# Optimization experiments

Measured on AMD Instinct MI355X. Metric: run time of the kernel, lower is better.

The kernel has to match this reference:

```python
import jax, jax.numpy as jnp
import numpy as np

N, E = 50000, 800000
HID, EDGE_DIM, HEADS = 128, 16, 4
C = HID // HEADS  # 32
NEG_SLOPE = 0.2  # GATv2Conv default negative_slope


def setup_inputs() -> dict:
    key = jax.random.key(0)
    ks = jax.random.split(key, 16)
    def glorot(k, shape):
        fan_in = shape[0]
        return jax.random.normal(k, shape, jnp.float32) / np.sqrt(fan_in)
    return {
        "x": jax.random.normal(ks[0], (N, HID), jnp.float32),
        "edge_index": jax.random.randint(ks[1], (2, E), 0, N, jnp.int64 if jax.config.jax_enable_x64 else jnp.int32),
        "edge_attr": jax.random.normal(ks[2], (E, EDGE_DIM), jnp.float32),
        # GATv2Conv params (lin_l, lin_r with bias; lin_edge bias-free; att; final bias)
        "Wl": glorot(ks[3], (HID, HID)),
        "bl": jnp.zeros((HID,), jnp.float32),
        "Wr": glorot(ks[4], (HID, HID)),
        "br": jnp.zeros((HID,), jnp.float32),
        "We": glorot(ks[5], (EDGE_DIM, HID)),
        "att": glorot(ks[6], (HEADS, C)),
        "bias_gat": jnp.zeros((HID,), jnp.float32),
        # RMSNorm weights
        "w_norm1": jnp.ones((HID,), jnp.float32),
        "w_norm2": jnp.ones((HID,), jnp.float32),
        # FFN params
        "ffn_w1": glorot(ks[7], (HID, 4 * HID)),
        "ffn_b1": jnp.zeros((4 * HID,), jnp.float32),
        "ffn_w2": glorot(ks[8], (4 * HID, HID)),
        "ffn_b2": jnp.zeros((HID,), jnp.float32),
    }


def rmsnorm(x, w):
    # torch.nn.RMSNorm with eps=None -> eps = finfo(dtype).eps
    eps = jnp.finfo(x.dtype).eps
    ms = jnp.mean(x * x, axis=-1, keepdims=True)
    return x * jax.lax.rsqrt(ms + eps) * w


def gatv2_conv(x, edge_index, edge_attr, Wl, bl, Wr, br, We, att, bias_gat):
    n = x.shape[0]
    h, c = att.shape
    xl = (x @ Wl + bl).reshape(n, h, c)   # source-side transform (x_j)
    xr = (x @ Wr + br).reshape(n, h, c)   # target-side transform (x_i)
    src, dst = edge_index[0], edge_index[1]
    e = (edge_attr @ We).reshape(-1, h, c)
    m = xl[src] + xr[dst] + e                       # [E, H, C] per-edge message pre-activation
    s = jnp.where(m > 0, m, NEG_SLOPE * m)          # LeakyReLU(0.2)
    logits = jnp.einsum('ehc,hc->eh', s, att)       # [E, H]
    # scatter-softmax over edges grouped by target node
    lmax = jax.ops.segment_max(logits, dst, num_segments=n)
    ex = jnp.exp(logits - lmax[dst])
    den = jax.ops.segment_sum(ex, dst, num_segments=n)
    alpha = ex / (den[dst] + 1e-16)                 # PyG softmax denominator guard
    out = jax.ops.segment_sum(alpha[..., None] * xl[src], dst, num_segments=n)
    return out.reshape(n, h * c) + bias_gat


def reference(x, edge_index, edge_attr, Wl, bl, Wr, br, We, att, bias_gat,
              w_norm1, w_norm2, ffn_w1, ffn_b1, ffn_w2, ffn_b2):
    x_attn = gatv2_conv(x, edge_index, edge_attr, Wl, bl, Wr, br, We, att, bias_gat)
    h = rmsnorm(x + x_attn, w_norm1)
    f = jax.nn.gelu(h @ ffn_w1 + ffn_b1, approximate=False) @ ffn_w2 + ffn_b2
    return rmsnorm(h + f, w_norm2)
```

## Files before the change

### kernel.cpp

```cpp
#include <hip/hip_runtime.h>

#define NN 50000
#define EE 800000

typedef unsigned short u16;

#define OFF_EAH  0u
#define OFF_XLH  6400000u
#define OFF_XRH  9600000u
#define OFF_SE   12800000u
#define OFF_CNT  14400000u
#define OFF_OFS  14450000u
#define OFF_WLRT 16000000u
#define OFF_W1T  16016384u
#define OFF_W2T  16049152u

#define RMS_EPS 1.1920928955078125e-7f

typedef float f32x4v __attribute__((ext_vector_type(4)));
typedef short s16x8 __attribute__((ext_vector_type(8)));
typedef _Float16 h16x2 __attribute__((ext_vector_type(2)));
typedef __fp16   g16x2 __attribute__((ext_vector_type(2)));

__device__ __forceinline__ f32x4v mfma16(s16x8 a, s16x8 b, f32x4v c) {
  return __builtin_amdgcn_mfma_f32_16x16x32_bf16(a, b, c, 0, 0, 0);
}
__device__ __forceinline__ u16 f2b(float f) {
  unsigned int u = __float_as_uint(f);
  unsigned int r = (u + 0x7fffu + ((u >> 16) & 1u)) >> 16;
  return (u16)r;
}
__device__ __forceinline__ u16 f2h(float f) {
  union { _Float16 h; u16 u; } x; x.h = (_Float16)f; return x.u;
}
__device__ __forceinline__ h16x2 pk(float a, float b) {
  union { g16x2 g; h16x2 h; } u; u.g = __builtin_amdgcn_cvt_pkrtz(a, b); return u.h;
}
__device__ __forceinline__ h16x2 u2h(unsigned int u) {
  union { unsigned int i; h16x2 h; } x; x.i = u; return x.h;
}
__device__ __forceinline__ unsigned int h2u(h16x2 h) {
  union { unsigned int i; h16x2 h; } x; x.h = h; return x.i;
}
__device__ __forceinline__ float fdot2(h16x2 a, h16x2 b, float c) {
  union { h16x2 h; g16x2 g; } ua, ub; ua.h = a; ub.h = b;
  return __builtin_amdgcn_fdot2(ua.g, ub.g, c, false);
}
__device__ __forceinline__ s16x8 ld_bf16x8_f32(const float* p) {
  float4 v0 = *(const float4*)p;
  float4 v1 = *(const float4*)(p + 4);
  s16x8 r;
  r[0] = (short)f2b(v0.x); r[1] = (short)f2b(v0.y);
  r[2] = (short)f2b(v0.z); r[3] = (short)f2b(v0.w);
  r[4] = (short)f2b(v1.x); r[5] = (short)f2b(v1.y);
  r[6] = (short)f2b(v1.z); r[7] = (short)f2b(v1.w);
  return r;
}
__device__ __forceinline__ int readlane_i32(int v, int lane) {
  return __builtin_amdgcn_readlane(v, lane);
}
__device__ __forceinline__ float gelu_fast(float x) {
  float x2 = x * x;
  float y = x * fmaf(0.07135481283f, x2, 1.5957691216f);
  float e = __expf(-y);
  return x * __builtin_amdgcn_rcpf(1.0f + e);
}

__global__ __launch_bounds__(256) void k_prep(const float* __restrict__ Wl, const float* __restrict__ Wr,
    const float* __restrict__ W1, const float* __restrict__ W2,
    int* __restrict__ cnt, u16* __restrict__ wlrt, u16* __restrict__ w1t, u16* __restrict__ w2t)
{
  int i = blockIdx.x * 256 + threadIdx.x;
  if (i < NN) cnt[i] = 0;
  if (i < 32768) {
    int n = i >> 7, k = i & 127;
    float v = (n < 128) ? Wl[k * 128 + n] : Wr[k * 128 + (n - 128)];
    wlrt[i] = f2b(v);
  }
  {
    int n = i >> 7, k = i & 127;
    w1t[i] = f2b(W1[k * 512 + n]);
  }
  {
    int n = i >> 9, k = i & 511;
    w2t[i] = f2b(W2[k * 128 + n]);
  }
}

__global__ __launch_bounds__(256) void k_hist(const int* __restrict__ ei, const float* __restrict__ eattr,
    int* __restrict__ cnt, unsigned int* __restrict__ eah)
{
  int e = blockIdx.x * 256 + threadIdx.x;
  if (e < EE) {
    atomicAdd(&cnt[ei[EE + e]], 1);
    const float4* src = (const float4*)(eattr + (size_t)e * 16);
    float4 v0 = src[0], v1 = src[1], v2 = src[2], v3 = src[3];
    uint4 o0, o1;
    o0.x = h2u(pk(v0.x, v0.y));
    o0.y = h2u(pk(v0.z, v0.w));
    o0.z = h2u(pk(v1.x, v1.y));
    o0.w = h2u(pk(v1.z, v1.w));
    o1.x = h2u(pk(v2.x, v2.y));
    o1.y = h2u(pk(v2.z, v2.w));
    o1.z = h2u(pk(v3.x, v3.y));
    o1.w = h2u(pk(v3.z, v3.w));
    uint4* dst = (uint4*)(eah + (size_t)e * 8);
    dst[0] = o0; dst[1] = o1;
  }
}

#define SCAN_PER 49
__global__ __launch_bounds__(1024) void k_scan(const int* __restrict__ cnt,
    int* __restrict__ offs, int* __restrict__ pos)
{
  __shared__ int wsum[16];
  int tid = threadIdx.x, lane = tid & 63, wv = tid >> 6;
  int base = tid * SCAN_PER;
  int v[SCAN_PER];
  int s = 0;
#pragma unroll
  for (int i = 0; i < SCAN_PER; ++i) {
    int idx = base + i;
    v[i] = (idx < NN) ? cnt[idx] : 0;
    s += v[i];
  }
  int x = s;
#pragma unroll
  for (int o = 1; o < 64; o <<= 1) {
    int y = __shfl_up(x, o);
    if (lane >= o) x += y;
  }
  if (lane == 63) wsum[wv] = x;
  __syncthreads();
  if (wv == 0) {
    int t = (lane < 16) ? wsum[lane] : 0;
#pragma unroll
    for (int o = 1; o < 16; o <<= 1) {
      int y = __shfl_up(t, o);
      if (lane >= o) t += y;
    }
    if (lane < 16) wsum[lane] = t;
  }
  __syncthreads();
  int wbase = (wv > 0) ? wsum[wv - 1] : 0;
  int run = x - s + wbase;
#pragma unroll
  for (int i = 0; i < SCAN_PER; ++i) {
    int idx = base + i;
    if (idx < NN) {
      pos[idx] = run;
      run += v[i];
      offs[idx + 1] = run;
    }
  }
  if (tid == 0) offs[0] = 0;
}

__global__ __launch_bounds__(256) void k_permute(const int* __restrict__ ei,
    int* __restrict__ pos, int2* __restrict__ se)
{
  int e = blockIdx.x * 256 + threadIdx.x;
  if (e < EE) {
    int slot = atomicAdd(&pos[ei[EE + e]], 1);
    se[slot] = make_int2(ei[e], e);
  }
}

__global__ __launch_bounds__(256) void k1_mfma(const float* __restrict__ x, const u16* __restrict__ wlrt,
    const float* __restrict__ bl, const float* __restrict__ br,
    u16* __restrict__ xlh, u16* __restrict__ xrh)
{
  int tid = threadIdx.x;
  int w = tid >> 6, lane = tid & 63;
  int quad = lane >> 4, l16 = lane & 15;
  int row0 = blockIdx.x * 32;
  int ko = quad * 8;
  f32x4v acc[2][4];
#pragma unroll
  for (int mt = 0; mt < 2; ++mt)
#pragma unroll
    for (int nt = 0; nt < 4; ++nt) acc[mt][nt] = (f32x4v){0.f, 0.f, 0.f, 0.f};
#pragma unroll
  for (int ks = 0; ks < 4; ++ks) {
    int k0 = ks * 32 + ko;
    s16x8 a[2];
#pragma unroll
    for (int mt = 0; mt < 2; ++mt) {
      int row = row0 + mt * 16 + l16; if (row >= NN) row = NN - 1;
      a[mt] = ld_bf16x8_f32(x + row * 128 + k0);
    }
#pragma unroll
    for (int nt = 0; nt < 4; ++nt) {
      int col = w * 64 + nt * 16 + l16;
      s16x8 b = *(const s16x8*)(wlrt + col * 128 + k0);
      acc[0][nt] = mfma16(a[0], b, acc[0][nt]);
      acc[1][nt] = mfma16(a[1], b, acc[1][nt]);
    }
  }
#pragma unroll
  for (int nt = 0; nt < 4; ++nt) {
    int col = w * 64 + nt * 16 + l16;
    bool isl = col < 128;
    float bias = isl ? bl[col] : br[col - 128];
    u16* dst = isl ? xlh : xrh;
    int cc = isl ? col : col - 128;
#pragma unroll
    for (int mt = 0; mt < 2; ++mt)
#pragma unroll
      for (int r = 0; r < 4; ++r) {
        int row = row0 + mt * 16 + quad * 4 + r;
        if (row < NN) dst[row * 128 + cc] = f2h(acc[mt][nt][r] + bias);
      }
  }
}

__global__ __launch_bounds__(256) void kA_attn(
    const int* __restrict__ offs, const int2* __restrict__ se,
    const unsigned int* __restrict__ eah,
    const float* __restrict__ att, const float* __restrict__ We,
    const u16* __restrict__ xlh, const u16* __restrict__ xrh,
    const float* __restrict__ x, const float* __restrict__ bg,
    const float* __restrict__ wn1, float* __restrict__ h)
{
  int l = threadIdx.x & 63;
  int wid = (blockIdx.x * blockDim.x + threadIdx.x) >> 6;
  int nw = (gridDim.x * blockDim.x) >> 6;
  int c0 = 2 * l;

  h16x2 wefA[8], wefB[8];
#pragma unroll
  for (int k = 0; k < 8; ++k) {
    wefA[k] = pk(We[(2 * k) * 128 + c0], We[(2 * k + 1) * 128 + c0]);
    wefB[k] = pk(We[(2 * k) * 128 + c0 + 1], We[(2 * k + 1) * 128 + c0 + 1]);
  }
  float a0 = att[c0], a1 = att[c0 + 1];
  h16x2 att06 = pk(0.6f * a0, 0.6f * a1);
  h16x2 att04 = pk(0.4f * a0, 0.4f * a1);

  for (int d = wid; d < NN; d += nw) {
    int start = offs[d];
    int deg = offs[d + 1] - start;
    h16x2 xr2 = u2h(*(const unsigned int*)(xrh + (size_t)d * 128 + c0));
    float mh = -1e30f, lh = 0.f, O0 = 0.f, O1 = 0.f;

    for (int base = 0; base < deg; base += 64) {
      bool act = (base + l) < deg;
      int idx = start + base + l;
      int2 sev = act ? se[idx] : make_int2(0, 0);
      int cnt = min(64, deg - base);
      for (int sub8 = 0; sub8 < cnt; sub8 += 8) {
        uint4 ea0[8], ea1[8];
#pragma unroll
        for (int j = 0; j < 8; ++j) {
          int eid = readlane_i32(sev.y, sub8 + j);
          const uint4* p8 = (const uint4*)(eah + (size_t)(unsigned)eid * 8);
          ea0[j] = p8[0]; ea1[j] = p8[1];
        }

        float p[8];
        unsigned int xlu[8];
#pragma unroll
        for (int j = 0; j < 8; ++j) {
          float ep0 = 0.f, ep1 = 0.f;
          ep0 = fdot2(u2h(ea0[j].x), wefA[0], ep0); ep1 = fdot2(u2h(ea0[j].x), wefB[0], ep1);
          ep0 = fdot2(u2h(ea0[j].y), wefA[1], ep0); ep1 = fdot2(u2h(ea0[j].y), wefB[1], ep1);
          ep0 = fdot2(u2h(ea0[j].z), wefA[2], ep0); ep1 = fdot2(u2h(ea0[j].z), wefB[2], ep1);
          ep0 = fdot2(u2h(ea0[j].w), wefA[3], ep0); ep1 = fdot2(u2h(ea0[j].w), wefB[3], ep1);
          ep0 = fdot2(u2h(ea1[j].x), wefA[4], ep0); ep1 = fdot2(u2h(ea1[j].x), wefB[4], ep1);
          ep0 = fdot2(u2h(ea1[j].y), wefA[5], ep0); ep1 = fdot2(u2h(ea1[j].y), wefB[5], ep1);
          ep0 = fdot2(u2h(ea1[j].z), wefA[6], ep0); ep1 = fdot2(u2h(ea1[j].z), wefB[6], ep1);
          ep0 = fdot2(u2h(ea1[j].w), wefA[7], ep0); ep1 = fdot2(u2h(ea1[j].w), wefB[7], ep1);

          int sr = readlane_i32(sev.x, sub8 + j);
          unsigned int xv = *(const unsigned int*)(xlh + (size_t)sr * 128 + c0);
          xlu[j] = xv;
          h16x2 m2 = u2h(xv) + xr2 + pk(ep0, ep1);
          h16x2 am = u2h(h2u(m2) & 0x7FFF7FFFu);
          p[j] = fdot2(m2, att06, fdot2(am, att04, 0.f));
        }
#pragma unroll
        for (int o = 1; o <= 8; o <<= 1) {
          p[0] += __shfl_xor(p[0], o); p[1] += __shfl_xor(p[1], o);
          p[2] += __shfl_xor(p[2], o); p[3] += __shfl_xor(p[3], o);
          p[4] += __shfl_xor(p[4], o); p[5] += __shfl_xor(p[5], o);
          p[6] += __shfl_xor(p[6], o); p[7] += __shfl_xor(p[7], o);
        }
#pragma unroll
        for (int j = 0; j < 8; ++j) if (sub8 + j >= cnt) p[j] = -1e30f;
        float nm = fmaxf(fmaxf(fmaxf(p[0], p[1]), fmaxf(p[2], p[3])),
                         fmaxf(fmaxf(p[4], p[5]), fmaxf(p[6], p[7])));
        nm = fmaxf(nm, mh);
        float sc = __expf(mh - nm);
#pragma unroll
        for (int j = 0; j < 8; ++j) p[j] = __expf(p[j] - nm);
        float bs = ((p[0] + p[1]) + (p[2] + p[3])) + ((p[4] + p[5]) + (p[6] + p[7]));
        lh = fmaf(lh, sc, bs);
        O0 *= sc; O1 *= sc;
        mh = nm;
#pragma unroll
        for (int j = 0; j < 8; ++j) {
          h16x2 xl2 = u2h(xlu[j]);
          O0 = fmaf(p[j], (float)xl2.x, O0);
          O1 = fmaf(p[j], (float)xl2.y, O1);
        }
      }
    }
    float inv = 1.f / (lh + 1e-16f);
    float2 xu = *(const float2*)(x + (size_t)d * 128 + c0);
    float2 bu = *(const float2*)(bg + c0);
    float v0 = O0 * inv + xu.x + bu.x;
    float v1 = O1 * inv + xu.y + bu.y;
    float ss = v0 * v0 + v1 * v1;
#pragma unroll
    for (int o = 1; o < 64; o <<= 1) ss += __shfl_xor(ss, o);
    float rr = rsqrtf(ss * (1.f / 128.f) + RMS_EPS);
    float2 wu = *(const float2*)(wn1 + c0);
    *(float2*)(h + (size_t)d * 128 + c0) = make_float2(v0 * rr * wu.x, v1 * rr * wu.y);
  }
}

__device__ __forceinline__ u16* tls_addr(u16* tls, int row, int col) {
  int byte = (row << 10) + (col << 1);
  byte ^= (row & 7) << 4;
  return (u16*)((char*)tls + byte);
}

__global__ __launch_bounds__(512) void k6_mfma(const float* h,
    const u16* __restrict__ w1t, const u16* __restrict__ w2t,
    const float* __restrict__ b1, const float* __restrict__ b2,
    const float* __restrict__ wn2, float* out)
{
  __shared__ u16 tls[32 * 512];
  int tid = threadIdx.x;
  int w = tid >> 6, lane = tid & 63;
  int quad = lane >> 4, l16 = lane & 15;
  int row0 = blockIdx.x * 32;
  int ko = quad * 8;

  f32x4v acc1[2][4];
#pragma unroll
  for (int mt = 0; mt < 2; ++mt)
#pragma unroll
    for (int nt = 0; nt < 4; ++nt) acc1[mt][nt] = (f32x4v){0.f, 0.f, 0.f, 0.f};
#pragma unroll
  for (int ks = 0; ks < 4; ++ks) {
    int k0 = ks * 32 + ko;
    s16x8 a[2];
#pragma unroll
    for (int mt = 0; mt < 2; ++mt) {
      int row = row0 + mt * 16 + l16; if (row >= NN) row = NN - 1;
      a[mt] = ld_bf16x8_f32(h + row * 128 + k0);
    }
#pragma unroll
    for (int nt = 0; nt < 4; ++nt) {
      int col = w * 64 + nt * 16 + l16;
      s16x8 b = *(const s16x8*)(w1t + col * 128 + k0);
      acc1[0][nt] = mfma16(a[0], b, acc1[0][nt]);
      acc1[1][nt] = mfma16(a[1], b, acc1[1][nt]);
    }
  }
#pragma unroll
  for (int nt = 0; nt < 4; ++nt) {
    int col = w * 64 + nt * 16 + l16;
    float bb = b1[col];
#pragma unroll
    for (int mt = 0; mt < 2; ++mt)
#pragma unroll
      for (int r = 0; r < 4; ++r) {
        float t = gelu_fast(acc1[mt][nt][r] + bb);
        *tls_addr(tls, mt * 16 + quad * 4 + r, col) = f2b(t);
      }
  }
  __syncthreads();

  f32x4v acc2[2];
  acc2[0] = (f32x4v){0.f, 0.f, 0.f, 0.f};
  acc2[1] = (f32x4v){0.f, 0.f, 0.f, 0.f};
  int col = w * 16 + l16;
  const u16* bptr = w2t + col * 512;
#pragma unroll
  for (int ks = 0; ks < 16; ++ks) {
    int k0 = ks * 32 + ko;
    s16x8 a2[2];
#pragma unroll
    for (int mt = 0; mt < 2; ++mt)
      a2[mt] = *(const s16x8*)tls_addr(tls, mt * 16 + l16, k0);
    s16x8 b = *(const s16x8*)(bptr + k0);
    acc2[0] = mfma16(a2[0], b, acc2[0]);
    acc2[1] = mfma16(a2[1], b, acc2[1]);
  }

  float bb2 = b2[col], wn = wn2[col];
  float ov[2][4];
#pragma unroll
  for (int mt = 0; mt < 2; ++mt)
#pragma unroll
    for (int r = 0; r < 4; ++r) {
      int row = row0 + mt * 16 + quad * 4 + r;
      int rowc = row < NN ? row : NN - 1;
      ov[mt][r] = h[rowc * 128 + col] + acc2[mt][r] + bb2;
    }
  __syncthreads();
  float (*red)[32] = (float (*)[32])(void*)tls;
#pragma unroll
  for (int mt = 0; mt < 2; ++mt)
#pragma unroll
    for (int r = 0; r < 4; ++r) {
      float q = ov[mt][r] * ov[mt][r];
      q += __shfl_xor(q, 1); q += __shfl_xor(q, 2);
      q += __shfl_xor(q, 4); q += __shfl_xor(q, 8);
      if (l16 == 0) red[w][mt * 16 + quad * 4 + r] = q;
    }
  __syncthreads();
#pragma unroll
  for (int mt = 0; mt < 2; ++mt)
#pragma unroll
    for (int r = 0; r < 4; ++r) {
      int rl = mt * 16 + quad * 4 + r;
      float tot = ((red[0][rl] + red[1][rl]) + (red[2][rl] + red[3][rl]))
                + ((red[4][rl] + red[5][rl]) + (red[6][rl] + red[7][rl]));
      float rr = rsqrtf(tot * (1.f / 128.f) + RMS_EPS);
      int row = row0 + rl;
      if (row < NN) {
        out[row * 128 + col] = ov[mt][r] * rr * wn;
      }
    }
}

extern "C" void kernel_launch(void* const* d_in, const int* in_sizes, int n_in,
                              void* d_out, int out_size, void* d_ws, size_t ws_size,
                              hipStream_t stream) {
  const float* x   = (const float*)d_in[0];
  const int*   ei  = (const int*)d_in[1];
  const float* ea  = (const float*)d_in[2];
  const float* Wl  = (const float*)d_in[3];
  const float* bl  = (const float*)d_in[4];
  const float* Wr  = (const float*)d_in[5];
  const float* br  = (const float*)d_in[6];
  const float* We  = (const float*)d_in[7];
  const float* att = (const float*)d_in[8];
  const float* bg  = (const float*)d_in[9];
  const float* wn1 = (const float*)d_in[10];
  const float* wn2 = (const float*)d_in[11];
  const float* W1  = (const float*)d_in[12];
  const float* b1  = (const float*)d_in[13];
  const float* W2  = (const float*)d_in[14];
  const float* b2  = (const float*)d_in[15];

  float* wsf = (float*)d_ws;
  int*   wsi = (int*)d_ws;

  unsigned int* eah = (unsigned int*)(wsf + OFF_EAH);
  u16* xlh    = (u16*)(wsf + OFF_XLH);
  u16* xrh    = (u16*)(wsf + OFF_XRH);
  int2* se    = (int2*)(wsf + OFF_SE);
  int* cnt    = wsi + OFF_CNT;
  int* pos    = wsi + OFF_CNT;
  int* offs   = wsi + OFF_OFS;
  u16* wlrt   = (u16*)(wsf + OFF_WLRT);
  u16* w1t    = (u16*)(wsf + OFF_W1T);
  u16* w2t    = (u16*)(wsf + OFF_W2T);
  float* hbuf = (float*)d_out;

  k_prep<<<256, 256, 0, stream>>>(Wl, Wr, W1, W2, cnt, wlrt, w1t, w2t);

  k_hist<<<(EE + 255) / 256, 256, 0, stream>>>(ei, ea, cnt, eah);
  k_scan<<<1, 1024, 0, stream>>>(cnt, offs, pos);
  k_permute<<<(EE + 255) / 256, 256, 0, stream>>>(ei, pos, se);

  k1_mfma<<<(NN + 31) / 32, 256, 0, stream>>>(x, wlrt, bl, br, xlh, xrh);

  kA_attn<<<4096, 256, 0, stream>>>(offs, se, eah, att, We, xlh, xrh, x, bg, wn1, hbuf);

  k6_mfma<<<(NN + 31) / 32, 512, 0, stream>>>(hbuf, w1t, w2t, b1, b2, wn2, (float*)d_out);
}
```

Baseline: 517.1 us.

## Merge permute with projection GEMM, double-buffer edge gathers, drop online-softmax max

```diff
diff --git a/kernel.cpp b/kernel.cpp
--- a/kernel.cpp
+++ b/kernel.cpp
@@ -156,24 +156,25 @@
   if (tid == 0) offs[0] = 0;
 }
 
-__global__ __launch_bounds__(256) void k_permute(const int* __restrict__ ei,
-    int* __restrict__ pos, int2* __restrict__ se)
-{
-  int e = blockIdx.x * 256 + threadIdx.x;
-  if (e < EE) {
-    int slot = atomicAdd(&pos[ei[EE + e]], 1);
-    se[slot] = make_int2(ei[e], e);
-  }
-}
-
-__global__ __launch_bounds__(256) void k1_mfma(const float* __restrict__ x, const u16* __restrict__ wlrt,
+#define PERM_BLOCKS 3125
+__global__ __launch_bounds__(256) void k_pk1(const int* __restrict__ ei,
+    int* __restrict__ pos, int2* __restrict__ se,
+    const float* __restrict__ x, const u16* __restrict__ wlrt,
     const float* __restrict__ bl, const float* __restrict__ br,
     u16* __restrict__ xlh, u16* __restrict__ xrh)
 {
+  if (blockIdx.x < PERM_BLOCKS) {
+    int e = blockIdx.x * 256 + threadIdx.x;
+    if (e < EE) {
+      int slot = atomicAdd(&pos[ei[EE + e]], 1);
+      se[slot] = make_int2(ei[e], e);
+    }
+    return;
+  }
   int tid = threadIdx.x;
   int w = tid >> 6, lane = tid & 63;
   int quad = lane >> 4, l16 = lane & 15;
-  int row0 = blockIdx.x * 32;
+  int row0 = (blockIdx.x - PERM_BLOCKS) * 32;
   int ko = quad * 8;
   f32x4v acc[2][4];
 #pragma unroll
@@ -241,40 +242,38 @@
     int start = offs[d];
     int deg = offs[d + 1] - start;
     h16x2 xr2 = u2h(*(const unsigned int*)(xrh + (size_t)d * 128 + c0));
-    float mh = -1e30f, lh = 0.f, O0 = 0.f, O1 = 0.f;
+    float lh = 0.f, O0 = 0.f, O1 = 0.f;
 
     for (int base = 0; base < deg; base += 64) {
       bool act = (base + l) < deg;
       int idx = start + base + l;
       int2 sev = act ? se[idx] : make_int2(0, 0);
       int cnt = min(64, deg - base);
-      for (int sub8 = 0; sub8 < cnt; sub8 += 8) {
-        uint4 ea0[8], ea1[8];
-#pragma unroll
-        for (int j = 0; j < 8; ++j) {
-          int eid = readlane_i32(sev.y, sub8 + j);
+
+      auto loadb = [&](int off, uint4* A, uint4* B, unsigned* X) {
+#pragma unroll
+        for (int j = 0; j < 4; ++j) {
+          int eid = readlane_i32(sev.y, off + j);
+          int sr  = readlane_i32(sev.x, off + j);
           const uint4* p8 = (const uint4*)(eah + (size_t)(unsigned)eid * 8);
-          ea0[j] = p8[0]; ea1[j] = p8[1];
+          A[j] = p8[0]; B[j] = p8[1];
+          X[j] = *(const unsigned int*)(xlh + (size_t)(unsigned)sr * 128 + c0);
         }
-
-        float p[8];
-        unsigned int xlu[8];
-#pragma unroll
-        for (int j = 0; j < 8; ++j) {
-          float ep0 = 0.f, ep1 = 0.f;
-          ep0 = fdot2(u2h(ea0[j].x), wefA[0], ep0); ep1 = fdot2(u2h(ea0[j].x), wefB[0], ep1);
-          ep0 = fdot2(u2h(ea0[j].y), wefA[1], ep0); ep1 = fdot2(u2h(ea0[j].y), wefB[1], ep1);
-          ep0 = fdot2(u2h(ea0[j].z), wefA[2], ep0); ep1 = fdot2(u2h(ea0[j].z), wefB[2], ep1);
-          ep0 = fdot2(u2h(ea0[j].w), wefA[3], ep0); ep1 = fdot2(u2h(ea0[j].w), wefB[3], ep1);
-          ep0 = fdot2(u2h(ea1[j].x), wefA[4], ep0); ep1 = fdot2(u2h(ea1[j].x), wefB[4], ep1);
-          ep0 = fdot2(u2h(ea1[j].y), wefA[5], ep0); ep1 = fdot2(u2h(ea1[j].y), wefB[5], ep1);
-          ep0 = fdot2(u2h(ea1[j].z), wefA[6], ep0); ep1 = fdot2(u2h(ea1[j].z), wefB[6], ep1);
-          ep0 = fdot2(u2h(ea1[j].w), wefA[7], ep0); ep1 = fdot2(u2h(ea1[j].w), wefB[7], ep1);
-
-          int sr = readlane_i32(sev.x, sub8 + j);
-          unsigned int xv = *(const unsigned int*)(xlh + (size_t)sr * 128 + c0);
-          xlu[j] = xv;
-          h16x2 m2 = u2h(xv) + xr2 + pk(ep0, ep1);
+      };
+      auto compute4 = [&](const uint4* A, const uint4* B, const unsigned* X, int sofs) {
+        float p[4];
+#pragma unroll
+        for (int j = 0; j < 4; ++j) {
+          float ep0 = fdot2(u2h(A[j].x), wefA[0], 0.f);
+          float ep1 = fdot2(u2h(A[j].x), wefB[0], 0.f);
+          ep0 = fdot2(u2h(A[j].y), wefA[1], ep0); ep1 = fdot2(u2h(A[j].y), wefB[1], ep1);
+          ep0 = fdot2(u2h(A[j].z), wefA[2], ep0); ep1 = fdot2(u2h(A[j].z), wefB[2], ep1);
+          ep0 = fdot2(u2h(A[j].w), wefA[3], ep0); ep1 = fdot2(u2h(A[j].w), wefB[3], ep1);
+          ep0 = fdot2(u2h(B[j].x), wefA[4], ep0); ep1 = fdot2(u2h(B[j].x), wefB[4], ep1);
+          ep0 = fdot2(u2h(B[j].y), wefA[5], ep0); ep1 = fdot2(u2h(B[j].y), wefB[5], ep1);
+          ep0 = fdot2(u2h(B[j].z), wefA[6], ep0); ep1 = fdot2(u2h(B[j].z), wefB[6], ep1);
+          ep0 = fdot2(u2h(B[j].w), wefA[7], ep0); ep1 = fdot2(u2h(B[j].w), wefB[7], ep1);
+          h16x2 m2 = u2h(X[j]) + xr2 + pk(ep0, ep1);
           h16x2 am = u2h(h2u(m2) & 0x7FFF7FFFu);
           p[j] = fdot2(m2, att06, fdot2(am, att04, 0.f));
         }
@@ -282,26 +281,28 @@
         for (int o = 1; o <= 8; o <<= 1) {
           p[0] += __shfl_xor(p[0], o); p[1] += __shfl_xor(p[1], o);
           p[2] += __shfl_xor(p[2], o); p[3] += __shfl_xor(p[3], o);
-          p[4] += __shfl_xor(p[4], o); p[5] += __shfl_xor(p[5], o);
-          p[6] += __shfl_xor(p[6], o); p[7] += __shfl_xor(p[7], o);
         }
 #pragma unroll
-        for (int j = 0; j < 8; ++j) if (sub8 + j >= cnt) p[j] = -1e30f;
-        float nm = fmaxf(fmaxf(fmaxf(p[0], p[1]), fmaxf(p[2], p[3])),
-                         fmaxf(fmaxf(p[4], p[5]), fmaxf(p[6], p[7])));
-        nm = fmaxf(nm, mh);
-        float sc = __expf(mh - nm);
-#pragma unroll
-        for (int j = 0; j < 8; ++j) p[j] = __expf(p[j] - nm);
-        float bs = ((p[0] + p[1]) + (p[2] + p[3])) + ((p[4] + p[5]) + (p[6] + p[7]));
-        lh = fmaf(lh, sc, bs);
-        O0 *= sc; O1 *= sc;
-        mh = nm;
-#pragma unroll
-        for (int j = 0; j < 8; ++j) {
-          h16x2 xl2 = u2h(xlu[j]);
+        for (int j = 0; j < 4; ++j)
+          p[j] = (sofs + j < cnt) ? __expf(p[j]) : 0.f;
+        lh += (p[0] + p[1]) + (p[2] + p[3]);
+#pragma unroll
+        for (int j = 0; j < 4; ++j) {
+          h16x2 xl2 = u2h(X[j]);
           O0 = fmaf(p[j], (float)xl2.x, O0);
           O1 = fmaf(p[j], (float)xl2.y, O1);
+        }
+      };
+
+      uint4 Aa[4], Ab[4]; unsigned Ax[4];
+      uint4 Ba[4], Bb[4]; unsigned Bx[4];
+      loadb(0, Aa, Ab, Ax);
+      for (int sub = 0; sub < cnt; sub += 8) {
+        if (sub + 4 < cnt) loadb(sub + 4, Ba, Bb, Bx);
+        compute4(Aa, Ab, Ax, sub);
+        if (sub + 4 < cnt) {
+          if (sub + 8 < cnt) loadb(sub + 8, Aa, Ab, Ax);
+          compute4(Ba, Bb, Bx, sub + 4);
         }
       }
     }
@@ -466,9 +467,8 @@
 
   k_hist<<<(EE + 255) / 256, 256, 0, stream>>>(ei, ea, cnt, eah);
   k_scan<<<1, 1024, 0, stream>>>(cnt, offs, pos);
-  k_permute<<<(EE + 255) / 256, 256, 0, stream>>>(ei, pos, se);
-
-  k1_mfma<<<(NN + 31) / 32, 256, 0, stream>>>(x, wlrt, bl, br, xlh, xrh);
+
+  k_pk1<<<PERM_BLOCKS + (NN + 31) / 32, 256, 0, stream>>>(ei, pos, se, x, wlrt, bl, br, xlh, xrh);
 
   kA_attn<<<4096, 256, 0, stream>>>(offs, se, eah, att, We, xlh, xrh, x, bg, wn1, hbuf);
 
```

Result: slower. 552.5 us (+6.9%).
